# Kernel optimization log

Measured on AMD Instinct MI355X. Metric: run time of the kernel, lower is better.

## Reference

```python
import jax, jax.numpy as jnp
import numpy as np

N = 100000   # nodes
E = 1600000  # edges
F_IN = 256   # input features
H = 64       # hidden
C = 40       # classes


def setup_inputs() -> dict:
    key = jax.random.key(0)
    k = jax.random.split(key, 5)
    x = jax.random.normal(k[0], (N, F_IN), dtype=jnp.float32)
    edge_index = jax.random.randint(k[1], (2, E), 0, N, dtype=jnp.int64)
    edge_attr = jax.random.uniform(k[2], (E,), dtype=jnp.float32)
    # GCNConv params (glorot-ish scale), biases zero like reset_parameters
    W1 = jax.random.normal(k[3], (F_IN, H), dtype=jnp.float32) * (1.0 / np.sqrt(F_IN))
    b1 = jnp.zeros((H,), dtype=jnp.float32)
    W2 = jax.random.normal(k[4], (H, C), dtype=jnp.float32) * (1.0 / np.sqrt(H))
    b2 = jnp.zeros((C,), dtype=jnp.float32)
    return {"x": x, "edge_index": edge_index, "edge_attr": edge_attr,
            "W1": W1, "b1": b1, "W2": W2, "b2": b2}


def _gcn_conv(x, W, b, src, dst, norm):
    h = x @ W                                   # [N, out]
    msg = h[src] * norm[:, None]                # gather + edge scale [E+N, out]
    out = jax.ops.segment_sum(msg, dst, num_segments=N)
    return out + b


def reference(x, edge_index, edge_attr, W1, b1, W2, b2):
    # gcn_norm: add self-loops (weight 1), symmetric D^-1/2 A D^-1/2
    loop = jnp.arange(N, dtype=edge_index.dtype)
    src = jnp.concatenate([edge_index[0], loop])
    dst = jnp.concatenate([edge_index[1], loop])
    w = jnp.concatenate([edge_attr, jnp.ones((N,), dtype=edge_attr.dtype)])
    deg = jax.ops.segment_sum(w, dst, num_segments=N)
    dinv = jnp.where(deg > 0, jax.lax.rsqrt(jnp.maximum(deg, 1e-30)), 0.0)
    norm = dinv[src] * w * dinv[dst]

    h = _gcn_conv(x, W1, b1, src, dst, norm)
    h = jax.nn.relu(h)                          # dropout is identity in eval mode
    h = _gcn_conv(h, W2, b2, src, dst, norm)
    return jax.nn.log_softmax(h, axis=1)
```

## Files before the change

kernel.cpp:

```cpp
#include <hip/hip_runtime.h>
#include <math.h>

#define NN   100000
#define NE   1600000
#define FIN  256
#define HID  64
#define NC   40
#define NBKT 391
#define EPB  6250
#define CAP  4608

typedef __attribute__((ext_vector_type(8))) short short8;
typedef __attribute__((ext_vector_type(4))) float float4v;

static __device__ __forceinline__ short f2bf(float f) {
    unsigned u = __float_as_uint(f);
    u += 0x7FFFu + ((u >> 16) & 1u);
    return (short)(u >> 16);
}
static __device__ __forceinline__ float bf2f(unsigned short b) {
    return __uint_as_float((unsigned)b << 16);
}

__global__ __launch_bounds__(256) void w1cvt_k(const float* __restrict__ W1,
                                               short* __restrict__ w1t) {
    int t = blockIdx.x * 256 + threadIdx.x;
    int k = t >> 6, n = t & 63;
    w1t[n * FIN + k] = f2bf(W1[k * HID + n]);
}

__global__ __launch_bounds__(256) void phaseA_k(const int* __restrict__ src,
                                                const int* __restrict__ dst,
                                                const float* __restrict__ w,
                                                int* __restrict__ cursor,
                                                int2* __restrict__ bucketbuf) {
    __shared__ int  hist[NBKT];
    __shared__ int  sc[512];
    __shared__ int  loc_base[NBKT];
    __shared__ int  loc_cur[NBKT];
    __shared__ int  gb[NBKT];
    __shared__ int2 buf[EPB];
    const int t  = threadIdx.x;
    const int e0 = blockIdx.x * EPB;

    for (int i = t; i < NBKT; i += 256) hist[i] = 0;
    __syncthreads();
    for (int i = t; i < EPB; i += 256) atomicAdd(&hist[dst[e0 + i] >> 8], 1);
    __syncthreads();
    sc[t]       = (t       < NBKT) ? hist[t]       : 0;
    sc[t + 256] = (t + 256 < NBKT) ? hist[t + 256] : 0;
    __syncthreads();
    for (int off = 1; off < 512; off <<= 1) {
        int a0 = (t >= off) ? sc[t - off] : 0;
        int a1 = sc[t + 256 - off];
        __syncthreads();
        sc[t] += a0; sc[t + 256] += a1;
        __syncthreads();
    }
    for (int i = t; i < NBKT; i += 256) {
        int base = sc[i] - hist[i];
        loc_base[i] = base;
        loc_cur[i]  = base;
        gb[i] = atomicAdd(&cursor[i * 16], hist[i]);
    }
    __syncthreads();
    for (int i = t; i < EPB; i += 256) {
        int e = e0 + i;
        int d = dst[e];
        int b = d >> 8;
        int p = atomicAdd(&loc_cur[b], 1);
        buf[p] = make_int2(src[e] | ((d & 255) << 17), __float_as_int(w[e]));
    }
    __syncthreads();
    for (int b = t; b < NBKT; b += 256) {
        int lb = loc_base[b], n = hist[b];
        int2* dstp = bucketbuf + (size_t)b * CAP + gb[b];
        for (int i = 0; i < n; ++i) dstp[i] = buf[lb + i];
    }
}

__global__ __launch_bounds__(512) void scanB_k(const int* __restrict__ cursor,
                                               int* __restrict__ bucketbase,
                                               int* __restrict__ row_start) {
    __shared__ int tmp[512];
    int t = threadIdx.x;
    int v = (t < NBKT) ? cursor[t * 16] : 0;
    tmp[t] = v;
    __syncthreads();
    for (int off = 1; off < 512; off <<= 1) {
        int add = (t >= off) ? tmp[t - off] : 0;
        __syncthreads(); tmp[t] += add; __syncthreads();
    }
    if (t < NBKT) bucketbase[t] = tmp[t] - v;
    if (t == 0) { bucketbase[NBKT] = NE; row_start[NN] = NE; }
}

__global__ __launch_bounds__(256) void phaseB_k(const int* __restrict__ bucketbase,
                                                const int2* __restrict__ bucketbuf,
                                                int2* __restrict__ e8,
                                                int* __restrict__ row_start,
                                                float* __restrict__ dinv) {
    __shared__ int2 buf[CAP];
    __shared__ int2 buf2[CAP];
    __shared__ int  hist2[256];
    __shared__ int  tmp[256];
    __shared__ int  base2[257];
    __shared__ int  cur2[256];
    const int b = blockIdx.x, t = threadIdx.x;
    const int g0   = bucketbase[b];
    const int cntb = bucketbase[b + 1] - g0;
    const int n0   = b * 256;
    const int nnb  = (NN - n0 < 256) ? (NN - n0) : 256;

    hist2[t] = 0;
    __syncthreads();
    const int2* bb = bucketbuf + (size_t)b * CAP;
    for (int i = t; i < cntb; i += 256) {
        int2 kv = bb[i];
        buf[i] = kv;
        atomicAdd(&hist2[kv.x >> 17], 1);
    }
    __syncthreads();
    int v = hist2[t];
    tmp[t] = v;
    __syncthreads();
    for (int off = 1; off < 256; off <<= 1) {
        int add = (t >= off) ? tmp[t - off] : 0;
        __syncthreads(); tmp[t] += add; __syncthreads();
    }
    int excl = tmp[t] - v;
    base2[t] = excl;
    cur2[t]  = excl;
    if (t == 0) base2[256] = cntb;
    if (t < nnb) row_start[n0 + t] = g0 + excl;
    __syncthreads();
    for (int i = t; i < cntb; i += 256) {
        int2 kv = buf[i];
        int d = kv.x >> 17;
        int p = atomicAdd(&cur2[d], 1);
        buf2[p] = make_int2(kv.x & 0x1FFFF, kv.y);
    }
    __syncthreads();
    for (int i = t; i < cntb; i += 256) e8[g0 + i] = buf2[i];
    if (t < nnb) {
        float s = 0.f;
        int j1 = base2[t + 1];
        for (int j = base2[t]; j < j1; ++j) s += __int_as_float(buf2[j].y);
        dinv[n0 + t] = rsqrtf(1.0f + s);
    }
}

__global__ __launch_bounds__(256) void gemm1_mfma_k(const float* __restrict__ x,
                                                    const short* __restrict__ w1t,
                                                    const float* __restrict__ dinv,
                                                    unsigned short* __restrict__ h1) {
    const int wave = threadIdx.x >> 6;
    const int lane = threadIdx.x & 63;
    const int m    = lane & 15;
    const int quad = lane >> 4;
    const int r0   = blockIdx.x * 64 + wave * 16;
    const int row  = r0 + m;
    const int rcl  = (row < NN) ? row : (NN - 1);
    const float* xrow = x + (size_t)rcl * FIN + quad * 8;

    float4v acc0 = {0.f,0.f,0.f,0.f}, acc1 = acc0, acc2 = acc0, acc3 = acc0;

#pragma unroll
    for (int kc = 0; kc < 8; ++kc) {
        const int kof = kc * 32 + quad * 8;
        float4 xa = *(const float4*)(xrow + kc * 32);
        float4 xb = *(const float4*)(xrow + kc * 32 + 4);
        short8 a;
        a[0] = f2bf(xa.x); a[1] = f2bf(xa.y); a[2] = f2bf(xa.z); a[3] = f2bf(xa.w);
        a[4] = f2bf(xb.x); a[5] = f2bf(xb.y); a[6] = f2bf(xb.z); a[7] = f2bf(xb.w);
        short8 b0 = *(const short8*)(w1t + (0 * 16 + m) * FIN + kof);
        short8 b1 = *(const short8*)(w1t + (1 * 16 + m) * FIN + kof);
        short8 b2 = *(const short8*)(w1t + (2 * 16 + m) * FIN + kof);
        short8 b3 = *(const short8*)(w1t + (3 * 16 + m) * FIN + kof);
        acc0 = __builtin_amdgcn_mfma_f32_16x16x32_bf16(a, b0, acc0, 0, 0, 0);
        acc1 = __builtin_amdgcn_mfma_f32_16x16x32_bf16(a, b1, acc1, 0, 0, 0);
        acc2 = __builtin_amdgcn_mfma_f32_16x16x32_bf16(a, b2, acc2, 0, 0, 0);
        acc3 = __builtin_amdgcn_mfma_f32_16x16x32_bf16(a, b3, acc3, 0, 0, 0);
    }
#pragma unroll
    for (int r = 0; r < 4; ++r) {
        int rr = r0 + quad * 4 + r;
        if (rr < NN) {
            float dv = dinv[rr];
            unsigned short* hp = h1 + (size_t)rr * HID + m;
            hp[0]  = (unsigned short)f2bf(acc0[r] * dv);
            hp[16] = (unsigned short)f2bf(acc1[r] * dv);
            hp[32] = (unsigned short)f2bf(acc2[r] * dv);
            hp[48] = (unsigned short)f2bf(acc3[r] * dv);
        }
    }
}

__global__ __launch_bounds__(256) void gatherA_k(const int* __restrict__ row_start,
                                                 const int2* __restrict__ e8,
                                                 const float* __restrict__ dinv,
                                                 const unsigned short* __restrict__ h,
                                                 const float* __restrict__ b1,
                                                 unsigned short* __restrict__ Rp) {
    const int v = blockIdx.x * 4 + (threadIdx.x >> 6);
    const int lane = threadIdx.x & 63;
    const int i0 = row_start[v], i1 = row_start[v + 1];
    float acc0 = 0.f, acc1 = 0.f, acc2 = 0.f, acc3 = 0.f;
    int i = i0;
    for (; i + 4 <= i1; i += 4) {
        int2 a = e8[i + 0], b = e8[i + 1], c = e8[i + 2], d = e8[i + 3];
        acc0 = fmaf(bf2f(h[(size_t)a.x * HID + lane]), __int_as_float(a.y), acc0);
        acc1 = fmaf(bf2f(h[(size_t)b.x * HID + lane]), __int_as_float(b.y), acc1);
        acc2 = fmaf(bf2f(h[(size_t)c.x * HID + lane]), __int_as_float(c.y), acc2);
        acc3 = fmaf(bf2f(h[(size_t)d.x * HID + lane]), __int_as_float(d.y), acc3);
    }
    for (; i < i1; ++i) {
        int2 a = e8[i];
        acc0 = fmaf(bf2f(h[(size_t)a.x * HID + lane]), __int_as_float(a.y), acc0);
    }
    const float dv = dinv[v];
    float r = (acc0 + acc1) + (acc2 + acc3);
    r = dv * (r + bf2f(h[(size_t)v * HID + lane]));
    r = fmaxf(r + b1[lane], 0.f);
    Rp[(size_t)v * HID + lane] = (unsigned short)f2bf(dv * r);
}

__global__ __launch_bounds__(256) void gatherB_k(const int* __restrict__ row_start,
                                                 const int2* __restrict__ e8,
                                                 const float* __restrict__ dinv,
                                                 const unsigned short* __restrict__ Rp,
                                                 float* __restrict__ agg2) {
    const int v = blockIdx.x * 4 + (threadIdx.x >> 6);
    const int lane = threadIdx.x & 63;
    const int i0 = row_start[v], i1 = row_start[v + 1];
    float acc0 = 0.f, acc1 = 0.f, acc2 = 0.f, acc3 = 0.f;
    int i = i0;
    for (; i + 4 <= i1; i += 4) {
        int2 a = e8[i + 0], b = e8[i + 1], c = e8[i + 2], d = e8[i + 3];
        acc0 = fmaf(bf2f(Rp[(size_t)a.x * HID + lane]), __int_as_float(a.y), acc0);
        acc1 = fmaf(bf2f(Rp[(size_t)b.x * HID + lane]), __int_as_float(b.y), acc1);
        acc2 = fmaf(bf2f(Rp[(size_t)c.x * HID + lane]), __int_as_float(c.y), acc2);
        acc3 = fmaf(bf2f(Rp[(size_t)d.x * HID + lane]), __int_as_float(d.y), acc3);
    }
    for (; i < i1; ++i) {
        int2 a = e8[i];
        acc0 = fmaf(bf2f(Rp[(size_t)a.x * HID + lane]), __int_as_float(a.y), acc0);
    }
    const float dv = dinv[v];
    float r = (acc0 + acc1) + (acc2 + acc3);
    agg2[(size_t)v * HID + lane] = dv * (r + bf2f(Rp[(size_t)v * HID + lane]));
}

__global__ __launch_bounds__(256) void gemm3_logsm_k(const float* __restrict__ agg2,
                                                     const float* __restrict__ W2,
                                                     const float* __restrict__ b2,
                                                     float* __restrict__ out) {
    __shared__ float w2s[HID * NC];
    __shared__ float b2s[NC];
    for (int i = threadIdx.x; i < HID * NC; i += 256) w2s[i] = W2[i];
    if (threadIdx.x < NC) b2s[threadIdx.x] = b2[threadIdx.x];
    __syncthreads();

    const int r = blockIdx.x * 256 + threadIdx.x;
    if (r >= NN) return;
    float acc[NC];
#pragma unroll
    for (int c = 0; c < NC; ++c) acc[c] = b2s[c];

    const float4* row4 = (const float4*)(agg2 + (size_t)r * HID);
    for (int kk = 0; kk < HID; kk += 4) {
        float4 v = row4[kk >> 2];
#pragma unroll
        for (int c = 0; c < NC; ++c) {
            acc[c] = fmaf(v.x, w2s[(kk + 0) * NC + c], acc[c]);
            acc[c] = fmaf(v.y, w2s[(kk + 1) * NC + c], acc[c]);
            acc[c] = fmaf(v.z, w2s[(kk + 2) * NC + c], acc[c]);
            acc[c] = fmaf(v.w, w2s[(kk + 3) * NC + c], acc[c]);
        }
    }
    float m = acc[0];
#pragma unroll
    for (int c = 1; c < NC; ++c) m = fmaxf(m, acc[c]);
    float s = 0.f;
#pragma unroll
    for (int c = 0; c < NC; ++c) s += __expf(acc[c] - m);
    float lg = m + __logf(s);
    float* outp = out + (size_t)r * NC;
#pragma unroll
    for (int c = 0; c < NC; c += 4)
        *(float4*)&outp[c] = make_float4(acc[c] - lg, acc[c+1] - lg, acc[c+2] - lg, acc[c+3] - lg);
}

extern "C" void kernel_launch(void* const* d_in, const int* in_sizes, int n_in,
                              void* d_out, int out_size, void* d_ws, size_t ws_size,
                              hipStream_t stream) {
    const float* x  = (const float*)d_in[0];
    const int*   ei = (const int*)d_in[1];
    const float* ea = (const float*)d_in[2];
    const float* W1 = (const float*)d_in[3];
    const float* b1 = (const float*)d_in[4];
    const float* W2 = (const float*)d_in[5];
    const float* b2 = (const float*)d_in[6];
    const int* src = ei;
    const int* dst = ei + NE;
    float* out = (float*)d_out;

    char* ws = (char*)d_ws;
    float* dinv       = (float*)(ws + 0);
    int*   row_start  = (int*)  (ws + 400000);
    int*   cursor     = (int*)  (ws + 800016);
    int*   bucketbase = (int*)  (ws + 825040);
    int2*  e8         = (int2*) (ws + 826608);
    unsigned short* h1 = (unsigned short*)(ws + 13626608);
    unsigned short* Rp = (unsigned short*)(ws + 26426608);
    float* agg2       = (float*)(ws + 39226608);
    short* w1t        = (short*)(ws + 64826608);
    int2*  bucketbuf  = (int2*)agg2;

    hipMemsetAsync(cursor, 0, 391 * 16 * sizeof(int), stream);

    w1cvt_k <<<64,   256, 0, stream>>>(W1, w1t);
    phaseA_k<<<256,  256, 0, stream>>>(src, dst, ea, cursor, bucketbuf);
    scanB_k <<<1,    512, 0, stream>>>(cursor, bucketbase, row_start);
    phaseB_k<<<NBKT, 256, 0, stream>>>(bucketbase, bucketbuf, e8, row_start, dinv);

    gemm1_mfma_k <<<(NN + 63) / 64, 256, 0, stream>>>(x, w1t, dinv, h1);
    gatherA_k    <<<NN / 4, 256, 0, stream>>>(row_start, e8, dinv, h1, b1, Rp);
    gatherB_k    <<<NN / 4, 256, 0, stream>>>(row_start, e8, dinv, Rp, agg2);
    gemm3_logsm_k<<<(NN + 255) / 256, 256, 0, stream>>>(agg2, W2, b2, out);
}
```

Before: 419.9 us.

## Partition each node's edges by source range so waves sweep sources together

phaseB now sorts each node's edges by an extra source-range key (source index >> 14, giving 7 ranges) and stores per-node cumulative offsets, packed as bytes, in a new qoff array. The gather kernels give each wave 13 nodes and walk the source ranges in order, so concurrent waves read the same region of the feature table. This is meant to improve L2 locality of the random row gathers. In exchange the kernels lose the 4-way unrolled independent loads, run a serial inner loop per node, re-read qoff and row_start on every pass, and use a fixed grid of 2048 blocks. The packed offsets are single bytes, so a node with 256 or more in-edges would overflow them.

```diff
diff --git a/kernel.cpp b/kernel.cpp
--- a/kernel.cpp
+++ b/kernel.cpp
@@ -9,6 +9,7 @@
 #define NBKT 391
 #define EPB  6250
 #define CAP  4608
+#define KPW  13
 
 typedef __attribute__((ext_vector_type(8))) short short8;
 typedef __attribute__((ext_vector_type(4))) float float4v;
@@ -99,53 +100,60 @@
                                                 const int2* __restrict__ bucketbuf,
                                                 int2* __restrict__ e8,
                                                 int* __restrict__ row_start,
-                                                float* __restrict__ dinv) {
-    __shared__ int2 buf[CAP];
+                                                float* __restrict__ dinv,
+                                                uint2* __restrict__ qoff) {
     __shared__ int2 buf2[CAP];
-    __shared__ int  hist2[256];
+    __shared__ int  hist2[2048];
+    __shared__ int  cur2[2048];
     __shared__ int  tmp[256];
-    __shared__ int  base2[257];
-    __shared__ int  cur2[256];
     const int b = blockIdx.x, t = threadIdx.x;
     const int g0   = bucketbase[b];
     const int cntb = bucketbase[b + 1] - g0;
     const int n0   = b * 256;
     const int nnb  = (NN - n0 < 256) ? (NN - n0) : 256;
 
-    hist2[t] = 0;
+    for (int i = t; i < 2048; i += 256) hist2[i] = 0;
     __syncthreads();
     const int2* bb = bucketbuf + (size_t)b * CAP;
     for (int i = t; i < cntb; i += 256) {
-        int2 kv = bb[i];
-        buf[i] = kv;
-        atomicAdd(&hist2[kv.x >> 17], 1);
-    }
-    __syncthreads();
-    int v = hist2[t];
-    tmp[t] = v;
+        int kx = bb[i].x;
+        atomicAdd(&hist2[((kx >> 17) << 3) | ((kx & 0x1FFFF) >> 14)], 1);
+    }
+    __syncthreads();
+    int hq[8];
+    int nodesum = 0;
+#pragma unroll
+    for (int q = 0; q < 8; ++q) { hq[q] = hist2[8 * t + q]; nodesum += hq[q]; }
+    tmp[t] = nodesum;
     __syncthreads();
     for (int off = 1; off < 256; off <<= 1) {
         int add = (t >= off) ? tmp[t - off] : 0;
         __syncthreads(); tmp[t] += add; __syncthreads();
     }
-    int excl = tmp[t] - v;
-    base2[t] = excl;
-    cur2[t]  = excl;
-    if (t == 0) base2[256] = cntb;
-    if (t < nnb) row_start[n0 + t] = g0 + excl;
+    const int nb = tmp[t] - nodesum;
+    {
+        unsigned lo = 0, hi = 0; int run = 0;
+#pragma unroll
+        for (int q = 0; q < 8; ++q) {
+            cur2[8 * t + q] = nb + run;
+            run += hq[q];
+            unsigned by = (unsigned)run & 255u;
+            if (q < 4) lo |= by << (8 * q); else hi |= by << (8 * (q - 4));
+        }
+        if (t < nnb) { row_start[n0 + t] = g0 + nb; qoff[n0 + t] = make_uint2(lo, hi); }
+    }
     __syncthreads();
     for (int i = t; i < cntb; i += 256) {
-        int2 kv = buf[i];
-        int d = kv.x >> 17;
-        int p = atomicAdd(&cur2[d], 1);
+        int2 kv = bb[i];
+        int key = ((kv.x >> 17) << 3) | ((kv.x & 0x1FFFF) >> 14);
+        int p = atomicAdd(&cur2[key], 1);
         buf2[p] = make_int2(kv.x & 0x1FFFF, kv.y);
     }
     __syncthreads();
     for (int i = t; i < cntb; i += 256) e8[g0 + i] = buf2[i];
     if (t < nnb) {
         float s = 0.f;
-        int j1 = base2[t + 1];
-        for (int j = base2[t]; j < j1; ++j) s += __int_as_float(buf2[j].y);
+        for (int j = nb; j < nb + nodesum; ++j) s += __int_as_float(buf2[j].y);
         dinv[n0 + t] = rsqrtf(1.0f + s);
     }
 }
@@ -196,59 +204,94 @@
     }
 }
 
-__global__ __launch_bounds__(256) void gatherA_k(const int* __restrict__ row_start,
-                                                 const int2* __restrict__ e8,
-                                                 const float* __restrict__ dinv,
-                                                 const unsigned short* __restrict__ h,
-                                                 const float* __restrict__ b1,
-                                                 unsigned short* __restrict__ Rp) {
-    const int v = blockIdx.x * 4 + (threadIdx.x >> 6);
+static __device__ __forceinline__ int qbyte(uint2 qo, int q) {
+    unsigned w = (q < 4) ? qo.x : qo.y;
+    return (int)((w >> (8 * (q & 3))) & 255u);
+}
+
+__global__ __launch_bounds__(256, 8) void gatherA_p(const int* __restrict__ row_start,
+                                                    const uint2* __restrict__ qoff,
+                                                    const int2* __restrict__ e8,
+                                                    const float* __restrict__ dinv,
+                                                    const unsigned short* __restrict__ h,
+                                                    const float* __restrict__ b1,
+                                                    unsigned short* __restrict__ Rp) {
+    const int wid  = blockIdx.x * 4 + (threadIdx.x >> 6);
     const int lane = threadIdx.x & 63;
-    const int i0 = row_start[v], i1 = row_start[v + 1];
-    float acc0 = 0.f, acc1 = 0.f, acc2 = 0.f, acc3 = 0.f;
-    int i = i0;
-    for (; i + 4 <= i1; i += 4) {
-        int2 a = e8[i + 0], b = e8[i + 1], c = e8[i + 2], d = e8[i + 3];
-        acc0 = fmaf(bf2f(h[(size_t)a.x * HID + lane]), __int_as_float(a.y), acc0);
-        acc1 = fmaf(bf2f(h[(size_t)b.x * HID + lane]), __int_as_float(b.y), acc1);
-        acc2 = fmaf(bf2f(h[(size_t)c.x * HID + lane]), __int_as_float(c.y), acc2);
-        acc3 = fmaf(bf2f(h[(size_t)d.x * HID + lane]), __int_as_float(d.y), acc3);
-    }
-    for (; i < i1; ++i) {
-        int2 a = e8[i];
-        acc0 = fmaf(bf2f(h[(size_t)a.x * HID + lane]), __int_as_float(a.y), acc0);
-    }
-    const float dv = dinv[v];
-    float r = (acc0 + acc1) + (acc2 + acc3);
-    r = dv * (r + bf2f(h[(size_t)v * HID + lane]));
-    r = fmaxf(r + b1[lane], 0.f);
-    Rp[(size_t)v * HID + lane] = (unsigned short)f2bf(dv * r);
-}
-
-__global__ __launch_bounds__(256) void gatherB_k(const int* __restrict__ row_start,
-                                                 const int2* __restrict__ e8,
-                                                 const float* __restrict__ dinv,
-                                                 const unsigned short* __restrict__ Rp,
-                                                 float* __restrict__ agg2) {
-    const int v = blockIdx.x * 4 + (threadIdx.x >> 6);
+    const int base = wid * KPW;
+    float acc[KPW];
+#pragma unroll
+    for (int j = 0; j < KPW; ++j) acc[j] = 0.f;
+
+    for (int q = 0; q < 7; ++q) {
+#pragma unroll
+        for (int j = 0; j < KPW; ++j) {
+            const int v = base + j;
+            if (v < NN) {
+                uint2 qo = qoff[v];
+                int e_end = qbyte(qo, q);
+                int e_beg = q ? qbyte(qo, q - 1) : 0;
+                int rs = row_start[v];
+                float a0 = 0.f;
+                for (int i = rs + e_beg; i < rs + e_end; ++i) {
+                    int2 a = e8[i];
+                    a0 = fmaf(bf2f(h[(size_t)a.x * HID + lane]), __int_as_float(a.y), a0);
+                }
+                acc[j] += a0;
+            }
+        }
+    }
+#pragma unroll
+    for (int j = 0; j < KPW; ++j) {
+        const int v = base + j;
+        if (v < NN) {
+            const float dv = dinv[v];
+            float r = dv * (acc[j] + bf2f(h[(size_t)v * HID + lane]));
+            r = fmaxf(r + b1[lane], 0.f);
+            Rp[(size_t)v * HID + lane] = (unsigned short)f2bf(dv * r);
+        }
+    }
+}
+
+__global__ __launch_bounds__(256, 8) void gatherB_p(const int* __restrict__ row_start,
+                                                    const uint2* __restrict__ qoff,
+                                                    const int2* __restrict__ e8,
+                                                    const float* __restrict__ dinv,
+                                                    const unsigned short* __restrict__ Rp,
+                                                    float* __restrict__ agg2) {
+    const int wid  = blockIdx.x * 4 + (threadIdx.x >> 6);
     const int lane = threadIdx.x & 63;
-    const int i0 = row_start[v], i1 = row_start[v + 1];
-    float acc0 = 0.f, acc1 = 0.f, acc2 = 0.f, acc3 = 0.f;
-    int i = i0;
-    for (; i + 4 <= i1; i += 4) {
-        int2 a = e8[i + 0], b = e8[i + 1], c = e8[i + 2], d = e8[i + 3];
-        acc0 = fmaf(bf2f(Rp[(size_t)a.x * HID + lane]), __int_as_float(a.y), acc0);
-        acc1 = fmaf(bf2f(Rp[(size_t)b.x * HID + lane]), __int_as_float(b.y), acc1);
-        acc2 = fmaf(bf2f(Rp[(size_t)c.x * HID + lane]), __int_as_float(c.y), acc2);
-        acc3 = fmaf(bf2f(Rp[(size_t)d.x * HID + lane]), __int_as_float(d.y), acc3);
-    }
-    for (; i < i1; ++i) {
-        int2 a = e8[i];
-        acc0 = fmaf(bf2f(Rp[(size_t)a.x * HID + lane]), __int_as_float(a.y), acc0);
-    }
-    const float dv = dinv[v];
-    float r = (acc0 + acc1) + (acc2 + acc3);
-    agg2[(size_t)v * HID + lane] = dv * (r + bf2f(Rp[(size_t)v * HID + lane]));
+    const int base = wid * KPW;
+    float acc[KPW];
+#pragma unroll
+    for (int j = 0; j < KPW; ++j) acc[j] = 0.f;
+
+    for (int q = 0; q < 7; ++q) {
+#pragma unroll
+        for (int j = 0; j < KPW; ++j) {
+            const int v = base + j;
+            if (v < NN) {
+                uint2 qo = qoff[v];
+                int e_end = qbyte(qo, q);
+                int e_beg = q ? qbyte(qo, q - 1) : 0;
+                int rs = row_start[v];
+                float a0 = 0.f;
+                for (int i = rs + e_beg; i < rs + e_end; ++i) {
+                    int2 a = e8[i];
+                    a0 = fmaf(bf2f(Rp[(size_t)a.x * HID + lane]), __int_as_float(a.y), a0);
+                }
+                acc[j] += a0;
+            }
+        }
+    }
+#pragma unroll
+    for (int j = 0; j < KPW; ++j) {
+        const int v = base + j;
+        if (v < NN) {
+            const float dv = dinv[v];
+            agg2[(size_t)v * HID + lane] = dv * (acc[j] + bf2f(Rp[(size_t)v * HID + lane]));
+        }
+    }
 }
 
 __global__ __launch_bounds__(256) void gemm3_logsm_k(const float* __restrict__ agg2,
@@ -315,6 +358,7 @@
     unsigned short* Rp = (unsigned short*)(ws + 26426608);
     float* agg2       = (float*)(ws + 39226608);
     short* w1t        = (short*)(ws + 64826608);
+    uint2* qoff       = (uint2*)(ws + 64859376);
     int2*  bucketbuf  = (int2*)agg2;
 
     hipMemsetAsync(cursor, 0, 391 * 16 * sizeof(int), stream);
@@ -322,10 +366,10 @@
     w1cvt_k <<<64,   256, 0, stream>>>(W1, w1t);
     phaseA_k<<<256,  256, 0, stream>>>(src, dst, ea, cursor, bucketbuf);
     scanB_k <<<1,    512, 0, stream>>>(cursor, bucketbase, row_start);
-    phaseB_k<<<NBKT, 256, 0, stream>>>(bucketbase, bucketbuf, e8, row_start, dinv);
+    phaseB_k<<<NBKT, 256, 0, stream>>>(bucketbase, bucketbuf, e8, row_start, dinv, qoff);
 
     gemm1_mfma_k <<<(NN + 63) / 64, 256, 0, stream>>>(x, w1t, dinv, h1);
-    gatherA_k    <<<NN / 4, 256, 0, stream>>>(row_start, e8, dinv, h1, b1, Rp);
-    gatherB_k    <<<NN / 4, 256, 0, stream>>>(row_start, e8, dinv, Rp, agg2);
+    gatherA_p    <<<2048, 256, 0, stream>>>(row_start, qoff, e8, dinv, h1, b1, Rp);
+    gatherB_p    <<<2048, 256, 0, stream>>>(row_start, qoff, e8, dinv, Rp, agg2);
     gemm3_logsm_k<<<(NN + 255) / 256, 256, 0, stream>>>(agg2, W2, b2, out);
 }
```

Result: slower. 666.8 us (+58.8%).
